# Optimization experiments

Measured on AMD Instinct MI355X. Metric: run time of the kernel, lower is better.

## Reference

```python
import jax, jax.numpy as jnp
import numpy as np
import math

N_NODES = 50000
N_EDGES = 800000
IN_DIM = 128
OUT_DIM = 64
TIME_DIM = 128


def setup_inputs() -> dict:
    key = jax.random.key(0)
    ks = jax.random.split(key, 9)
    return {
        "node_feats": jax.random.normal(ks[0], (N_NODES, IN_DIM), dtype=jnp.float32),
        "time_diff": jax.random.uniform(ks[1], (N_EDGES,), dtype=jnp.float32),
        "src": jax.random.randint(ks[2], (N_EDGES,), 0, N_NODES, dtype=jnp.int32),
        "dst": jax.random.randint(ks[3], (N_EDGES,), 0, N_NODES, dtype=jnp.int32),
        "W": jax.random.normal(ks[4], (OUT_DIM, IN_DIM), dtype=jnp.float32) * 0.05,
        "Wv": jax.random.normal(ks[5], (OUT_DIM, IN_DIM), dtype=jnp.float32) * 0.05,
        "omega": jax.random.normal(ks[6], (TIME_DIM // 2,), dtype=jnp.float32),
        "Wt": jax.random.normal(ks[7], (OUT_DIM, TIME_DIM), dtype=jnp.float32) * 0.05,
        "a": jax.random.normal(ks[8], (3 * OUT_DIM,), dtype=jnp.float32) * 0.05,
    }


def reference(node_feats, time_diff, src, dst, W, Wv, omega, Wt, a):
    N = node_feats.shape[0]
    d = W.shape[0]  # out_dim
    time_dim = 2 * omega.shape[0]

    # gather + linear projections per edge
    h_src = node_feats[src] @ W.T          # [E, d]
    h_dst = node_feats[dst] @ W.T          # [E, d]
    v_src = node_feats[src] @ Wv.T         # [E, d]

    # temporal encoding: interleaved sin/cos of t * omega, scaled by sqrt(1/dim)
    ang = time_diff[:, None] * omega[None, :]                       # [E, dim/2]
    pe = jnp.stack([jnp.sin(ang), jnp.cos(ang)], axis=-1)
    pe = pe.reshape(ang.shape[0], time_dim) * jnp.float32(math.sqrt(1.0 / time_dim))
    t_emb = pe @ Wt.T                                               # [E, d]

    # attn_fc(concat([h_src, h_dst, t_emb])) == split dot products (same math, no big concat)
    e = h_src @ a[:d] + h_dst @ a[d:2 * d] + t_emb @ a[2 * d:]      # [E]
    e = jnp.where(e > 0, e, 0.2 * e)  # LeakyReLU(0.2)

    # edge_softmax: softmax over incoming edges of each destination node
    m = jax.ops.segment_max(e, dst, num_segments=N)
    ex = jnp.exp(e - m[dst])
    den = jax.ops.segment_sum(ex, dst, num_segments=N)
    alpha = ex / den[dst]  # dropout is identity in eval mode

    # weighted message scatter-sum aggregation
    msg = v_src * alpha[:, None]                                    # [E, d]
    return jax.ops.segment_sum(msg, dst, num_segments=N)            # [N, d]
```

## Files before the change

kernel.cpp:

```cpp
#include <hip/hip_runtime.h>
#include <hip/hip_bf16.h>
#include <hip/hip_fp16.h>
#include <math.h>

#define IN_DIM   128
#define OUT_DIM  64
#define THALF    64
#define PE_SCALE 0.08838834764831845f
#define TBL      2048

typedef __attribute__((ext_vector_type(8))) short  short8;
typedef __attribute__((ext_vector_type(4))) float  f32x4;

__device__ inline unsigned short bf16_rne(float x) {
    unsigned u = __float_as_uint(x);
    return (unsigned short)((u + 0x7FFFu + ((u >> 16) & 1u)) >> 16);
}

__global__ __launch_bounds__(256) void k_params_pack(
    const float* __restrict__ W, const float* __restrict__ Wt,
    const float* __restrict__ a, const float* __restrict__ Wv,
    float* __restrict__ atv, unsigned short* __restrict__ Bp)
{
    __shared__ float saW1[IN_DIM], saW2[IN_DIM];
    int k = threadIdx.x;
    if (k < IN_DIM) {
        float x1 = 0.f, x2 = 0.f, x3 = 0.f;
        for (int j = 0; j < OUT_DIM; ++j) {
            float wj = W[j * IN_DIM + k];
            x1 += a[j] * wj;
            x2 += a[OUT_DIM + j] * wj;
            x3 += a[2 * OUT_DIM + j] * Wt[j * IN_DIM + k];
        }
        saW1[k] = x1; saW2[k] = x2; atv[k] = x3;
    }
    __syncthreads();
    for (int i = threadIdx.x; i < 5 * 4 * 64 * 8; i += 256) {
        int j    = i & 7;
        int lane = (i >> 3) & 63;
        int k0i  = (i >> 9) & 3;
        int t    = i >> 11;
        int kk = k0i * 32 + (lane >> 4) * 8 + j;
        int n  = lane & 15;
        float val;
        if (t < 4)      val = Wv[(t * 16 + n) * IN_DIM + kk];
        else            val = (n == 0) ? saW1[kk] : (n == 1) ? saW2[kk] : 0.f;
        Bp[i] = bf16_rne(val);
    }
}

__global__ __launch_bounds__(256) void k_gtab(
    const float* __restrict__ omega,
    const float* __restrict__ atv,
    float* __restrict__ gtab,
    int* __restrict__ cnt, int N)
{
    int idx = blockIdx.x * 256 + threadIdx.x;
    if (idx <= TBL) {
        float t = (float)idx * (1.0f / TBL);
        float acc = 0.f;
#pragma unroll
        for (int i = 0; i < THALF; ++i) {
            float sp, cp;
            __sincosf(t * omega[i], &sp, &cp);
            acc += sp * atv[2 * i] + cp * atv[2 * i + 1];
        }
        gtab[idx] = acc;
    }
    for (int i = idx; i < N; i += gridDim.x * 256) cnt[i] = 0;
}

__global__ __launch_bounds__(256) void k_node_mfma(
    const float* __restrict__ feats,
    const unsigned short* __restrict__ Bp,
    unsigned short* __restrict__ vb,
    float* __restrict__ s1,
    float* __restrict__ s2,
    int N)
{
    int gwave = (blockIdx.x * 256 + threadIdx.x) >> 6;
    int lane  = threadIdx.x & 63;
    int ntiles = (N + 15) >> 4;
    if (gwave >= ntiles) return;
    int row = lane & 15, quad = lane >> 4;
    int nodeA = gwave * 16 + row;
    int nodeL = nodeA < N ? nodeA : N - 1;

    const float* arow = feats + (size_t)nodeL * IN_DIM + quad * 8;
    short8 afrag[4];
#pragma unroll
    for (int k0i = 0; k0i < 4; ++k0i) {
        float4 fa = *(const float4*)(arow + k0i * 32);
        float4 fb = *(const float4*)(arow + k0i * 32 + 4);
        union { unsigned u[4]; short8 s; } cv;
        cv.u[0] = (__float_as_uint(fa.x) >> 16) | (__float_as_uint(fa.y) & 0xFFFF0000u);
        cv.u[1] = (__float_as_uint(fa.z) >> 16) | (__float_as_uint(fa.w) & 0xFFFF0000u);
        cv.u[2] = (__float_as_uint(fb.x) >> 16) | (__float_as_uint(fb.y) & 0xFFFF0000u);
        cv.u[3] = (__float_as_uint(fb.z) >> 16) | (__float_as_uint(fb.w) & 0xFFFF0000u);
        afrag[k0i] = cv.s;
    }

    const short8* B8 = (const short8*)Bp;
    f32x4 acc[5];
#pragma unroll
    for (int t = 0; t < 5; ++t) acc[t] = (f32x4){0.f, 0.f, 0.f, 0.f};
#pragma unroll
    for (int t = 0; t < 5; ++t) {
#pragma unroll
        for (int k0i = 0; k0i < 4; ++k0i)
            acc[t] = __builtin_amdgcn_mfma_f32_16x16x32_bf16(
                afrag[k0i], B8[(t * 4 + k0i) * 64 + lane], acc[t], 0, 0, 0);
    }

    int col = lane & 15;
    int baseNode = gwave * 16 + quad * 4;
#pragma unroll
    for (int r = 0; r < 4; ++r) {
        int nd = baseNode + r;
        if (nd < N) {
            unsigned short* vr = vb + (size_t)nd * OUT_DIM + col;
#pragma unroll
            for (int t = 0; t < 4; ++t) vr[t * 16] = bf16_rne(acc[t][r]);
            if (col == 0)      s1[nd] = acc[4][r];
            else if (col == 1) s2[nd] = acc[4][r];
        }
    }
}

__global__ __launch_bounds__(256) void k_logits_rank(
    const float* __restrict__ tdiff,
    const int* __restrict__ src,
    const int* __restrict__ dst,
    const float* __restrict__ gtab,
    const float* __restrict__ s1,
    const float* __restrict__ s2,
    int* __restrict__ cnt,
    int2* __restrict__ rp,
    int E)
{
    int e = blockIdx.x * blockDim.x + threadIdx.x;
    if (e >= E) return;
    int s = src[e], d = dst[e];
    int rk = atomicAdd(cnt + d, 1);
    float a1 = s1[s];
    float a2 = s2[d];
    float t = tdiff[e];

    float x = t * (float)TBL;
    int i0 = (int)x;
    i0 = i0 < 0 ? 0 : (i0 > TBL - 1 ? TBL - 1 : i0);
    float fr = x - (float)i0;
    float g0 = gtab[i0], g1 = gtab[i0 + 1];
    float ev = a1 + a2 + PE_SCALE * (g0 + fr * (g1 - g0));
    ev = ev > 0.f ? ev : 0.2f * ev;

    unsigned pw = ((unsigned)s << 16) | (unsigned)__half_as_ushort(__float2half(ev));
    rp[e] = make_int2(rk, (int)pw);
}

__global__ __launch_bounds__(256) void k_scan1(const int* __restrict__ cnt,
                                               int* __restrict__ offs,
                                               int* __restrict__ bsum, int N)
{
    __shared__ int lds[256];
    int b = blockIdx.x, t = threadIdx.x;
    int base = b * 1024 + t * 4;
    int v0 = (base + 0 < N) ? cnt[base + 0] : 0;
    int v1 = (base + 1 < N) ? cnt[base + 1] : 0;
    int v2 = (base + 2 < N) ? cnt[base + 2] : 0;
    int v3 = (base + 3 < N) ? cnt[base + 3] : 0;
    int s = v0 + v1 + v2 + v3;
    lds[t] = s;
    __syncthreads();
    for (int off = 1; off < 256; off <<= 1) {
        int tmp = (t >= off) ? lds[t - off] : 0;
        __syncthreads();
        lds[t] += tmp;
        __syncthreads();
    }
    int ex = lds[t] - s;
    if (base + 0 < N) offs[base + 0] = ex;
    ex += v0;
    if (base + 1 < N) offs[base + 1] = ex;
    ex += v1;
    if (base + 2 < N) offs[base + 2] = ex;
    ex += v2;
    if (base + 3 < N) offs[base + 3] = ex;
    if (t == 255) bsum[b] = lds[255];
}

__global__ __launch_bounds__(256) void k_scan3(int* __restrict__ offs,
                                               const int* __restrict__ bsum,
                                               int N, int E)
{
    int i = blockIdx.x * 256 + threadIdx.x;
    if (i < N) {
        int c = i >> 10;
        int p = 0;
        for (int j = 0; j < c; ++j) p += bsum[j];
        offs[i] += p;
    }
    if (i == 0) offs[N] = E;
}

__global__ __launch_bounds__(256) void k_scatter(
    const int* __restrict__ dst,
    const int2* __restrict__ rp,
    const int* __restrict__ offs,
    unsigned* __restrict__ payload,
    int E)
{
    int e = blockIdx.x * blockDim.x + threadIdx.x;
    if (e >= E) return;
    int2 v = rp[e];
    payload[offs[dst[e]] + v.x] = (unsigned)v.y;
}

__global__ __launch_bounds__(256) void k_aggregate(
    const int* __restrict__ offs,
    const unsigned* __restrict__ payload,
    const unsigned short* __restrict__ vb,
    float* __restrict__ out,
    int N)
{
    int wid  = (blockIdx.x * blockDim.x + threadIdx.x) >> 6;
    int lane = threadIdx.x & 63;
    if (wid >= N) return;
    int beg = offs[wid];
    int deg = offs[wid + 1] - beg;
    int g8 = lane >> 3, r = lane & 7;

    float acc[8];
#pragma unroll
    for (int i = 0; i < 8; ++i) acc[i] = 0.f;
    float den = 0.f;

    for (int base = 0; base < deg; base += 64) {
        int cl = deg - base; if (cl > 64) cl = 64;
        bool valid = lane < cl;
        unsigned pl = valid ? payload[beg + base + lane] : 0u;
        float ex = valid ? __expf(__half2float(__ushort_as_half((unsigned short)(pl & 0xFFFFu)))) : 0.f;
        int   sv = valid ? (int)(pl >> 16) : 0;

        float sum = ex;
#pragma unroll
        for (int off = 32; off; off >>= 1) sum += __shfl_xor(sum, off, 64);
        den += sum;

        int rounds = (cl + 15) >> 4;
        for (int j = 0; j < rounds; ++j) {
            int i0 = j * 16 + g8;
            int i1 = i0 + 8;
            float e0 = __shfl(ex, i0, 64);
            int   s0 = __shfl(sv, i0, 64);
            float e1 = __shfl(ex, i1, 64);
            int   s1v = __shfl(sv, i1, 64);
            uint4 w0 = *((const uint4*)(vb + (size_t)s0 * OUT_DIM) + r);
            uint4 w1 = *((const uint4*)(vb + (size_t)s1v * OUT_DIM) + r);
            acc[0] += e0 * __uint_as_float(w0.x << 16)         + e1 * __uint_as_float(w1.x << 16);
            acc[1] += e0 * __uint_as_float(w0.x & 0xFFFF0000u) + e1 * __uint_as_float(w1.x & 0xFFFF0000u);
            acc[2] += e0 * __uint_as_float(w0.y << 16)         + e1 * __uint_as_float(w1.y << 16);
            acc[3] += e0 * __uint_as_float(w0.y & 0xFFFF0000u) + e1 * __uint_as_float(w1.y & 0xFFFF0000u);
            acc[4] += e0 * __uint_as_float(w0.z << 16)         + e1 * __uint_as_float(w1.z << 16);
            acc[5] += e0 * __uint_as_float(w0.z & 0xFFFF0000u) + e1 * __uint_as_float(w1.z & 0xFFFF0000u);
            acc[6] += e0 * __uint_as_float(w0.w << 16)         + e1 * __uint_as_float(w1.w << 16);
            acc[7] += e0 * __uint_as_float(w0.w & 0xFFFF0000u) + e1 * __uint_as_float(w1.w & 0xFFFF0000u);
        }
    }

#pragma unroll
    for (int i = 0; i < 8; ++i) {
        acc[i] += __shfl_xor(acc[i], 8, 64);
        acc[i] += __shfl_xor(acc[i], 16, 64);
        acc[i] += __shfl_xor(acc[i], 32, 64);
    }

    if (g8 == 0) {
        float inv = (deg > 0) ? 1.f / den : 0.f;
        float* o = out + (size_t)wid * OUT_DIM + r * 8;
        *(float4*)(o)     = make_float4(acc[0] * inv, acc[1] * inv, acc[2] * inv, acc[3] * inv);
        *(float4*)(o + 4) = make_float4(acc[4] * inv, acc[5] * inv, acc[6] * inv, acc[7] * inv);
    }
}

extern "C" void kernel_launch(void* const* d_in, const int* in_sizes, int n_in,
                              void* d_out, int out_size, void* d_ws, size_t ws_size,
                              hipStream_t stream) {
    const float* feats = (const float*)d_in[0];
    const float* tdiff = (const float*)d_in[1];
    const int*   src   = (const int*)d_in[2];
    const int*   dst   = (const int*)d_in[3];
    const float* W     = (const float*)d_in[4];
    const float* Wv    = (const float*)d_in[5];
    const float* omega = (const float*)d_in[6];
    const float* Wt    = (const float*)d_in[7];
    const float* a     = (const float*)d_in[8];
    float* out = (float*)d_out;

    int N = in_sizes[0] / IN_DIM;
    int E = in_sizes[1];

    int offs_elems = ((N + 1 + 3) / 4) * 4;
    float* ws      = (float*)d_ws;
    unsigned short* vb = (unsigned short*)ws;
    float* s1      = ws + (size_t)N * 32;
    float* s2      = s1 + N;
    int2*  rp      = (int2*)(s2 + N);
    unsigned* payload = (unsigned*)(rp + E);
    int*   cnt     = (int*)(payload + E);
    int*   offs    = cnt + N;
    int*   bsum    = offs + offs_elems;
    float* atv     = (float*)(bsum + 64);
    float* gtab    = atv + IN_DIM;
    unsigned short* Bp = (unsigned short*)(gtab + TBL + 1);

    int nb = (N + 1023) / 1024;
    int ntiles = (N + 15) / 16;

    k_params_pack<<<1, 256, 0, stream>>>(W, Wt, a, Wv, atv, Bp);
    k_gtab<<<64, 256, 0, stream>>>(omega, atv, gtab, cnt, N);
    k_node_mfma<<<(ntiles * 64 + 255) / 256, 256, 0, stream>>>(feats, Bp, vb, s1, s2, N);
    k_logits_rank<<<(E + 255) / 256, 256, 0, stream>>>(tdiff, src, dst, gtab, s1, s2, cnt, rp, E);
    k_scan1<<<nb, 256, 0, stream>>>(cnt, offs, bsum, N);
    k_scan3<<<(N + 255) / 256, 256, 0, stream>>>(offs, bsum, N, E);
    k_scatter<<<(E + 255) / 256, 256, 0, stream>>>(dst, rp, offs, payload, E);
    long long tot = (long long)N * OUT_DIM;
    k_aggregate<<<(int)((tot + 255) / 256), 256, 0, stream>>>(offs, payload, vb, out, N);
}
```

Baseline: 191.8 us.

## Merge prep kernels, drop scan3 via atomic block prefixes, vectorize edge kernels

Fuses the parameter-pack and sin/cos table kernels into a single 64-block prep kernel. Each block recomputes the time-weight vector into shared memory, and only block 0 packs the MFMA weights. The separate scan fix-up kernel is removed: scan1 atomically adds each block total into a per-chunk prefix array, and scatter and aggregate add that prefix on the fly. The logits and scatter kernels now handle two edges per thread with vector loads and stores. This removes two launches and a pass over offsets, at the cost of extra prefix lookups and atomics.

After: 191.5 us. About the same (-0.2%).

```diff
diff --git a/kernel.cpp b/kernel.cpp
--- a/kernel.cpp
+++ b/kernel.cpp
@@ -17,57 +17,62 @@
     return (unsigned short)((u + 0x7FFFu + ((u >> 16) & 1u)) >> 16);
 }
 
-__global__ __launch_bounds__(256) void k_params_pack(
+__global__ __launch_bounds__(256) void k_prep(
     const float* __restrict__ W, const float* __restrict__ Wt,
     const float* __restrict__ a, const float* __restrict__ Wv,
-    float* __restrict__ atv, unsigned short* __restrict__ Bp)
-{
+    const float* __restrict__ omega,
+    float* __restrict__ gtab, unsigned short* __restrict__ Bp,
+    int* __restrict__ cnt, int* __restrict__ pref, int N)
+{
+    __shared__ float satv[IN_DIM];
     __shared__ float saW1[IN_DIM], saW2[IN_DIM];
-    int k = threadIdx.x;
-    if (k < IN_DIM) {
-        float x1 = 0.f, x2 = 0.f, x3 = 0.f;
-        for (int j = 0; j < OUT_DIM; ++j) {
-            float wj = W[j * IN_DIM + k];
-            x1 += a[j] * wj;
-            x2 += a[OUT_DIM + j] * wj;
-            x3 += a[2 * OUT_DIM + j] * Wt[j * IN_DIM + k];
-        }
-        saW1[k] = x1; saW2[k] = x2; atv[k] = x3;
+    int t = threadIdx.x;
+    if (t < IN_DIM) {
+        float x3 = 0.f;
+        for (int j = 0; j < OUT_DIM; ++j)
+            x3 += a[2 * OUT_DIM + j] * Wt[j * IN_DIM + t];
+        satv[t] = x3;
+        if (blockIdx.x == 0) {
+            float x1 = 0.f, x2 = 0.f;
+            for (int j = 0; j < OUT_DIM; ++j) {
+                float wj = W[j * IN_DIM + t];
+                x1 += a[j] * wj;
+                x2 += a[OUT_DIM + j] * wj;
+            }
+            saW1[t] = x1; saW2[t] = x2;
+        }
     }
     __syncthreads();
-    for (int i = threadIdx.x; i < 5 * 4 * 64 * 8; i += 256) {
-        int j    = i & 7;
-        int lane = (i >> 3) & 63;
-        int k0i  = (i >> 9) & 3;
-        int t    = i >> 11;
-        int kk = k0i * 32 + (lane >> 4) * 8 + j;
-        int n  = lane & 15;
-        float val;
-        if (t < 4)      val = Wv[(t * 16 + n) * IN_DIM + kk];
-        else            val = (n == 0) ? saW1[kk] : (n == 1) ? saW2[kk] : 0.f;
-        Bp[i] = bf16_rne(val);
-    }
-}
-
-__global__ __launch_bounds__(256) void k_gtab(
-    const float* __restrict__ omega,
-    const float* __restrict__ atv,
-    float* __restrict__ gtab,
-    int* __restrict__ cnt, int N)
-{
-    int idx = blockIdx.x * 256 + threadIdx.x;
+
+    int idx = blockIdx.x * 256 + t;
     if (idx <= TBL) {
-        float t = (float)idx * (1.0f / TBL);
+        float tt = (float)idx * (1.0f / TBL);
         float acc = 0.f;
 #pragma unroll
         for (int i = 0; i < THALF; ++i) {
             float sp, cp;
-            __sincosf(t * omega[i], &sp, &cp);
-            acc += sp * atv[2 * i] + cp * atv[2 * i + 1];
+            __sincosf(tt * omega[i], &sp, &cp);
+            acc += sp * satv[2 * i] + cp * satv[2 * i + 1];
         }
         gtab[idx] = acc;
     }
+    if (idx < 64) pref[idx] = 0;
     for (int i = idx; i < N; i += gridDim.x * 256) cnt[i] = 0;
+
+    if (blockIdx.x == 0) {
+        for (int i = t; i < 5 * 4 * 64 * 8; i += 256) {
+            int j    = i & 7;
+            int lane = (i >> 3) & 63;
+            int k0i  = (i >> 9) & 3;
+            int tt   = i >> 11;
+            int kk = k0i * 32 + (lane >> 4) * 8 + j;
+            int n  = lane & 15;
+            float val;
+            if (tt < 4)     val = Wv[(tt * 16 + n) * IN_DIM + kk];
+            else            val = (n == 0) ? saW1[kk] : (n == 1) ? saW2[kk] : 0.f;
+            Bp[i] = bf16_rne(val);
+        }
+    }
 }
 
 __global__ __launch_bounds__(256) void k_node_mfma(
@@ -138,29 +143,53 @@
     int2* __restrict__ rp,
     int E)
 {
-    int e = blockIdx.x * blockDim.x + threadIdx.x;
+    int e = (blockIdx.x * blockDim.x + threadIdx.x) * 2;
     if (e >= E) return;
-    int s = src[e], d = dst[e];
-    int rk = atomicAdd(cnt + d, 1);
-    float a1 = s1[s];
-    float a2 = s2[d];
-    float t = tdiff[e];
-
-    float x = t * (float)TBL;
-    int i0 = (int)x;
-    i0 = i0 < 0 ? 0 : (i0 > TBL - 1 ? TBL - 1 : i0);
-    float fr = x - (float)i0;
-    float g0 = gtab[i0], g1 = gtab[i0 + 1];
-    float ev = a1 + a2 + PE_SCALE * (g0 + fr * (g1 - g0));
-    ev = ev > 0.f ? ev : 0.2f * ev;
-
-    unsigned pw = ((unsigned)s << 16) | (unsigned)__half_as_ushort(__float2half(ev));
-    rp[e] = make_int2(rk, (int)pw);
+    if (e + 1 < E) {
+        int2   s2v = *(const int2*)(src + e);
+        int2   d2v = *(const int2*)(dst + e);
+        float2 t2v = *(const float2*)(tdiff + e);
+        int rk0 = atomicAdd(cnt + d2v.x, 1);
+        int rk1 = atomicAdd(cnt + d2v.y, 1);
+        float a10 = s1[s2v.x], a11 = s1[s2v.y];
+        float a20 = s2[d2v.x], a21 = s2[d2v.y];
+
+        float x0 = t2v.x * (float)TBL;
+        int i0 = (int)x0;
+        i0 = i0 < 0 ? 0 : (i0 > TBL - 1 ? TBL - 1 : i0);
+        float fr0 = x0 - (float)i0;
+        float ev0 = a10 + a20 + PE_SCALE * (gtab[i0] + fr0 * (gtab[i0 + 1] - gtab[i0]));
+        ev0 = ev0 > 0.f ? ev0 : 0.2f * ev0;
+
+        float x1 = t2v.y * (float)TBL;
+        int i1 = (int)x1;
+        i1 = i1 < 0 ? 0 : (i1 > TBL - 1 ? TBL - 1 : i1);
+        float fr1 = x1 - (float)i1;
+        float ev1 = a11 + a21 + PE_SCALE * (gtab[i1] + fr1 * (gtab[i1 + 1] - gtab[i1]));
+        ev1 = ev1 > 0.f ? ev1 : 0.2f * ev1;
+
+        unsigned pw0 = ((unsigned)s2v.x << 16) | (unsigned)__half_as_ushort(__float2half(ev0));
+        unsigned pw1 = ((unsigned)s2v.y << 16) | (unsigned)__half_as_ushort(__float2half(ev1));
+        int4 o = make_int4(rk0, (int)pw0, rk1, (int)pw1);
+        *(int4*)(rp + e) = o;
+    } else {
+        int s = src[e], d = dst[e];
+        int rk = atomicAdd(cnt + d, 1);
+        float a1 = s1[s], a2 = s2[d];
+        float x = tdiff[e] * (float)TBL;
+        int i0 = (int)x;
+        i0 = i0 < 0 ? 0 : (i0 > TBL - 1 ? TBL - 1 : i0);
+        float fr = x - (float)i0;
+        float ev = a1 + a2 + PE_SCALE * (gtab[i0] + fr * (gtab[i0 + 1] - gtab[i0]));
+        ev = ev > 0.f ? ev : 0.2f * ev;
+        unsigned pw = ((unsigned)s << 16) | (unsigned)__half_as_ushort(__float2half(ev));
+        rp[e] = make_int2(rk, (int)pw);
+    }
 }
 
 __global__ __launch_bounds__(256) void k_scan1(const int* __restrict__ cnt,
                                                int* __restrict__ offs,
-                                               int* __restrict__ bsum, int N)
+                                               int* __restrict__ pref, int N)
 {
     __shared__ int lds[256];
     int b = blockIdx.x, t = threadIdx.x;
@@ -186,48 +215,46 @@
     if (base + 2 < N) offs[base + 2] = ex;
     ex += v2;
     if (base + 3 < N) offs[base + 3] = ex;
-    if (t == 255) bsum[b] = lds[255];
-}
-
-__global__ __launch_bounds__(256) void k_scan3(int* __restrict__ offs,
-                                               const int* __restrict__ bsum,
-                                               int N, int E)
-{
-    int i = blockIdx.x * 256 + threadIdx.x;
-    if (i < N) {
-        int c = i >> 10;
-        int p = 0;
-        for (int j = 0; j < c; ++j) p += bsum[j];
-        offs[i] += p;
-    }
-    if (i == 0) offs[N] = E;
+    int total = lds[255];
+    if (t > b && t < (int)gridDim.x) atomicAdd(pref + t, total);
 }
 
 __global__ __launch_bounds__(256) void k_scatter(
     const int* __restrict__ dst,
     const int2* __restrict__ rp,
     const int* __restrict__ offs,
+    const int* __restrict__ pref,
     unsigned* __restrict__ payload,
     int E)
 {
-    int e = blockIdx.x * blockDim.x + threadIdx.x;
+    int e = (blockIdx.x * blockDim.x + threadIdx.x) * 2;
     if (e >= E) return;
-    int2 v = rp[e];
-    payload[offs[dst[e]] + v.x] = (unsigned)v.y;
+    if (e + 1 < E) {
+        int2 d2 = *(const int2*)(dst + e);
+        int4 v2 = *(const int4*)(rp + e);
+        payload[offs[d2.x] + pref[d2.x >> 10] + v2.x] = (unsigned)v2.y;
+        payload[offs[d2.y] + pref[d2.y >> 10] + v2.z] = (unsigned)v2.w;
+    } else {
+        int d = dst[e];
+        int2 v = rp[e];
+        payload[offs[d] + pref[d >> 10] + v.x] = (unsigned)v.y;
+    }
 }
 
 __global__ __launch_bounds__(256) void k_aggregate(
     const int* __restrict__ offs,
+    const int* __restrict__ pref,
     const unsigned* __restrict__ payload,
     const unsigned short* __restrict__ vb,
     float* __restrict__ out,
-    int N)
+    int N, int E)
 {
     int wid  = (blockIdx.x * blockDim.x + threadIdx.x) >> 6;
     int lane = threadIdx.x & 63;
     if (wid >= N) return;
-    int beg = offs[wid];
-    int deg = offs[wid + 1] - beg;
+    int beg = offs[wid] + pref[wid >> 10];
+    int end = (wid + 1 < N) ? (offs[wid + 1] + pref[(wid + 1) >> 10]) : E;
+    int deg = end - beg;
     int g8 = lane >> 3, r = lane & 7;
 
     float acc[8];
@@ -309,21 +336,19 @@
     unsigned* payload = (unsigned*)(rp + E);
     int*   cnt     = (int*)(payload + E);
     int*   offs    = cnt + N;
-    int*   bsum    = offs + offs_elems;
-    float* atv     = (float*)(bsum + 64);
-    float* gtab    = atv + IN_DIM;
+    int*   pref    = offs + offs_elems;
+    float* gtab    = (float*)(pref + 64);
     unsigned short* Bp = (unsigned short*)(gtab + TBL + 1);
 
     int nb = (N + 1023) / 1024;
     int ntiles = (N + 15) / 16;
-
-    k_params_pack<<<1, 256, 0, stream>>>(W, Wt, a, Wv, atv, Bp);
-    k_gtab<<<64, 256, 0, stream>>>(omega, atv, gtab, cnt, N);
+    int ethreads = (E + 1) / 2;
+
+    k_prep<<<64, 256, 0, stream>>>(W, Wt, a, Wv, omega, gtab, Bp, cnt, pref, N);
     k_node_mfma<<<(ntiles * 64 + 255) / 256, 256, 0, stream>>>(feats, Bp, vb, s1, s2, N);
-    k_logits_rank<<<(E + 255) / 256, 256, 0, stream>>>(tdiff, src, dst, gtab, s1, s2, cnt, rp, E);
-    k_scan1<<<nb, 256, 0, stream>>>(cnt, offs, bsum, N);
-    k_scan3<<<(N + 255) / 256, 256, 0, stream>>>(offs, bsum, N, E);
-    k_scatter<<<(E + 255) / 256, 256, 0, stream>>>(dst, rp, offs, payload, E);
+    k_logits_rank<<<(ethreads + 255) / 256, 256, 0, stream>>>(tdiff, src, dst, gtab, s1, s2, cnt, rp, E);
+    k_scan1<<<nb, 256, 0, stream>>>(cnt, offs, pref, N);
+    k_scatter<<<(ethreads + 255) / 256, 256, 0, stream>>>(dst, rp, offs, pref, payload, E);
     long long tot = (long long)N * OUT_DIM;
-    k_aggregate<<<(int)((tot + 255) / 256), 256, 0, stream>>>(offs, payload, vb, out, N);
-}
+    k_aggregate<<<(int)((tot + 255) / 256), 256, 0, stream>>>(offs, pref, payload, vb, out, N, E);
+}
```
